# Optimization experiments

Measured on AMD Instinct MI355X. Metric: run time of the kernel, lower is better.

Reference implementation:

```python
import jax, jax.numpy as jnp
import numpy as np

BLOCK = 32


def _dct_constants(bs):
    # Replicates get_dct_constants + the sorting/reshaping done in DCTEncoderLayer.__init__
    x, y = np.meshgrid(np.arange(bs), np.arange(bs), indexing='xy')
    basis = np.zeros((bs, bs, bs, bs), dtype=np.float32)
    mag = np.zeros((bs, bs), dtype=np.float64)
    fac = np.zeros((bs, bs), dtype=np.float32)
    for v in range(bs):
        for u in range(bs):
            xb = np.cos((2 * x + 1) * u * np.pi / (2 * bs))
            yb = np.cos((2 * y + 1) * v * np.pi / (2 * bs))
            basis[v, u] = (xb * yb).astype(np.float32)
            mag[v, u] = np.linalg.norm(np.array([v, u], dtype=np.int64))
            c_v = 1 / np.sqrt(2) if v == 0 else 1.0
            c_u = 1 / np.sqrt(2) if u == 0 else 1.0
            fac[v, u] = c_u * c_v
    kernels = basis.reshape(-1, bs, bs)
    factors = fac.reshape(-1)
    idx = np.argsort(mag.reshape(-1))  # same default argsort as the torch module
    return kernels[idx].astype(np.float32), factors[idx].astype(np.float32)


def setup_inputs() -> dict:
    key = jax.random.key(0)
    rgb = jax.random.uniform(key, (32, 3, 512, 512), dtype=jnp.float32)
    kernels, factors = _dct_constants(BLOCK)
    return {
        "rgb_images_batch": rgb,
        "kernels": jnp.asarray(kernels),   # [K=bs^2, bs, bs], sorted by freq magnitude
        "factors": jnp.asarray(factors),   # [K]
    }


def _rgb_to_ycbcr(rgb):
    # kornia.color.rgb_to_ycbcr (delta = 0.5)
    r, g, b = rgb[:, 0], rgb[:, 1], rgb[:, 2]
    y = 0.299 * r + 0.587 * g + 0.114 * b
    cb = (b - y) * 0.564 + 0.5
    cr = (r - y) * 0.713 + 0.5
    return jnp.stack([y, cb, cr], axis=1)  # [B,3,H,W]


def reference(rgb_images_batch, kernels, factors):
    bs = BLOCK
    B, C, H, W = rgb_images_batch.shape
    nh, nw = H // bs, W // bs
    ycbcr = 2.0 * _rgb_to_ycbcr(rgb_images_batch) - 1.0            # [B,3,H,W]
    # non-overlapping blocks: [B,3,nh,nw,bs,bs]
    blocks = ycbcr.reshape(B, 3, nh, bs, nw, bs).transpose(0, 1, 2, 4, 3, 5)
    # stride=bs conv2d with dense DCT basis kernels == per-block contraction
    coeffs = jnp.einsum('bcmnxy,kxy->bckmn', blocks, kernels)      # [B,3,K,nh,nw]
    scale = (2.0 / bs) * factors                                   # [K]
    coeffs = coeffs * scale[None, None, :, None, None]
    # torch.cat([y, cb, cr], dim=1) -> [B, 3*K, nh, nw]
    return coeffs.reshape(B, 3 * bs * bs, nh, nw)
```

## Files before the change

kernel.cpp:

```cpp
#include <hip/hip_runtime.h>
#include <math.h>


typedef __bf16 bf16x8 __attribute__((ext_vector_type(8)));
typedef float  f32x4  __attribute__((ext_vector_type(4)));

#define PI_F 3.14159265358979323846f

__device__ __forceinline__ unsigned short f2bf(float f) {
    union { float f; unsigned u; } v; v.f = f;
    unsigned u = v.u;
    u += 0x7fffu + ((u >> 16) & 1u);
    return (unsigned short)(u >> 16);
}

__global__ __launch_bounds__(256) void setup_kernel(const float* __restrict__ kern,
                                                    const float* __restrict__ factors,
                                                    unsigned short* __restrict__ Cbf,
                                                    int* __restrict__ P,
                                                    float* __restrict__ S) {
    int k = blockIdx.x * 256 + threadIdx.x;
    int i = k & 31, t = k >> 5;
    Cbf[k] = f2bf(cosf((float)((2 * i + 1) * t) * (PI_F / 64.f)));

    float k00 = kern[(size_t)k * 1024];
    float rv  = kern[(size_t)k * 1024 + 32] / k00;
    float ru  = kern[(size_t)k * 1024 + 1]  / k00;
    float cv2 = fminf(fmaxf((rv + 3.f) * 0.25f, 0.f), 1.f);
    float cu2 = fminf(fmaxf((ru + 3.f) * 0.25f, 0.f), 1.f);
    int v = __float2int_rn(acosf(sqrtf(cv2)) * (64.f / PI_F));
    int u = __float2int_rn(acosf(sqrtf(cu2)) * (64.f / PI_F));
    P[v * 32 + u] = k;
    S[k] = factors[k] * (2.f / 32.f);
}

__global__ __launch_bounds__(512, 2) void dct_fused(const float* __restrict__ rgb,
                                                    const unsigned short* __restrict__ Cbf,
                                                    const int* __restrict__ P,
                                                    const float* __restrict__ S,
                                                    float* __restrict__ out) {
    __shared__ __align__(16) unsigned char Tls[32 * 1280];

    const int tid  = threadIdx.x;
    const int lane = tid & 63;
    const int w    = tid >> 6;
    const int quad = lane >> 4;
    const int l15  = lane & 15;
    const int b    = blockIdx.x >> 4;
    const int m    = blockIdx.x & 15;

    union { bf16x8 v; unsigned short s[8]; } af0, af1;
    af0.v = *(const bf16x8*)(Cbf + l15 * 32 + quad * 8);
    af1.v = *(const bf16x8*)(Cbf + (16 + l15) * 32 + quad * 8);

    const f32x4 zero = {0.f, 0.f, 0.f, 0.f};
    f32x4 d[3][2][4];

    const float* rbase = rgb + (size_t)b * 786432 + (size_t)l15 * 32 + (size_t)quad * 8;
#pragma unroll
    for (int xi = 0; xi < 4; ++xi) {
        const int x = w * 4 + xi;
        const float* p = rbase + (size_t)(m * 32 + x) * 512;
        float4 R0 = *(const float4*)(p);
        float4 R1 = *(const float4*)(p + 4);
        float4 G0 = *(const float4*)(p + 262144);
        float4 G1 = *(const float4*)(p + 262148);
        float4 B0 = *(const float4*)(p + 524288);
        float4 B1 = *(const float4*)(p + 524292);
        float R[8]  = {R0.x, R0.y, R0.z, R0.w, R1.x, R1.y, R1.z, R1.w};
        float G[8]  = {G0.x, G0.y, G0.z, G0.w, G1.x, G1.y, G1.z, G1.w};
        float Bv[8] = {B0.x, B0.y, B0.z, B0.w, B1.x, B1.y, B1.z, B1.w};
        union { bf16x8 v; unsigned short s[8]; } fy, fcb, fcr;
#pragma unroll
        for (int e = 0; e < 8; ++e) {
            float y = 0.299f * R[e] + 0.587f * G[e] + 0.114f * Bv[e];
            fy.s[e]  = f2bf(2.f * y - 1.f);
            fcb.s[e] = f2bf(1.128f * (Bv[e] - y));
            fcr.s[e] = f2bf(1.426f * (R[e] - y));
        }
        d[0][0][xi] = __builtin_amdgcn_mfma_f32_16x16x32_bf16(af0.v, fy.v,  zero, 0, 0, 0);
        d[0][1][xi] = __builtin_amdgcn_mfma_f32_16x16x32_bf16(af1.v, fy.v,  zero, 0, 0, 0);
        d[1][0][xi] = __builtin_amdgcn_mfma_f32_16x16x32_bf16(af0.v, fcb.v, zero, 0, 0, 0);
        d[1][1][xi] = __builtin_amdgcn_mfma_f32_16x16x32_bf16(af1.v, fcb.v, zero, 0, 0, 0);
        d[2][0][xi] = __builtin_amdgcn_mfma_f32_16x16x32_bf16(af0.v, fcr.v, zero, 0, 0, 0);
        d[2][1][xi] = __builtin_amdgcn_mfma_f32_16x16x32_bf16(af1.v, fcr.v, zero, 0, 0, 0);
    }

    const size_t obase0 = (size_t)(b * 3) * 262144 + (size_t)m * 16 + (size_t)l15;
#pragma unroll 1
    for (int c = 0; c < 3; ++c) {
#pragma unroll
        for (int fh = 0; fh < 2; ++fh)
#pragma unroll
            for (int r = 0; r < 4; ++r) {
                const int f1 = fh * 16 + quad * 4 + r;
                ushort4 pk;
                pk.x = f2bf(d[c][fh][0][r]);
                pk.y = f2bf(d[c][fh][1][r]);
                pk.z = f2bf(d[c][fh][2][r]);
                pk.w = f2bf(d[c][fh][3][r]);
                *(ushort4*)(Tls + f1 * 1280 + l15 * 80 + w * 8) = pk;
            }
        __syncthreads();

        const size_t obase = obase0 + (size_t)c * 262144;
#pragma unroll
        for (int i = 0; i < 4; ++i) {
            const int f1 = w * 4 + i;
            bf16x8 bfr = *(const bf16x8*)(Tls + f1 * 1280 + l15 * 80 + quad * 16);
#pragma unroll
            for (int uh = 0; uh < 2; ++uh) {
                f32x4 d2 = __builtin_amdgcn_mfma_f32_16x16x32_bf16(
                    uh ? af1.v : af0.v, bfr, zero, 0, 0, 0);
                const int f2b = uh * 16 + quad * 4;
#pragma unroll
                for (int r = 0; r < 4; ++r) {
                    const int kk = P[(f2b + r) * 32 + f1];
                    out[obase + (size_t)kk * 256] = d2[r] * S[kk];
                }
            }
        }
        __syncthreads();
    }
}

extern "C" void kernel_launch(void* const* d_in, const int* in_sizes, int n_in,
                              void* d_out, int out_size, void* d_ws, size_t ws_size,
                              hipStream_t stream) {
    const float* rgb     = (const float*)d_in[0];
    const float* kern    = (const float*)d_in[1];
    const float* factors = (const float*)d_in[2];
    float* out = (float*)d_out;

    unsigned short* Cbf = (unsigned short*)d_ws;
    int*   P = (int*)((char*)d_ws + 8192);
    float* S = (float*)((char*)d_ws + 12288);

    setup_kernel<<<4, 256, 0, stream>>>(kern, factors, Cbf, P, S);
    dct_fused<<<512, 512, 0, stream>>>(rgb, Cbf, P, S, out);
}
```

Baseline: 234.5 us.

## Defer first-pass MFMAs per channel, pack index/scale table, raise occupancy

The kernel now keeps the converted bf16 input fragments in registers and runs the first-pass MFMAs per channel inside the channel loop, instead of holding all 24 f32x4 accumulators live. This lowers register pressure so launch bounds can request 4 blocks per SM instead of 2. The permutation index and scale are packed into one int2 table, so each output needs one dependent load instead of two. The block-row mapping is also swizzled. The risks are more MFMA work sitting on the store path, and the shared-memory footprint limiting the extra occupancy.

```diff
diff --git a/kernel.cpp b/kernel.cpp
--- a/kernel.cpp
+++ b/kernel.cpp
@@ -17,8 +17,7 @@
 __global__ __launch_bounds__(256) void setup_kernel(const float* __restrict__ kern,
                                                     const float* __restrict__ factors,
                                                     unsigned short* __restrict__ Cbf,
-                                                    int* __restrict__ P,
-                                                    float* __restrict__ S) {
+                                                    int2* __restrict__ T2) {
     int k = blockIdx.x * 256 + threadIdx.x;
     int i = k & 31, t = k >> 5;
     Cbf[k] = f2bf(cosf((float)((2 * i + 1) * t) * (PI_F / 64.f)));
@@ -30,14 +29,13 @@
     float cu2 = fminf(fmaxf((ru + 3.f) * 0.25f, 0.f), 1.f);
     int v = __float2int_rn(acosf(sqrtf(cv2)) * (64.f / PI_F));
     int u = __float2int_rn(acosf(sqrtf(cu2)) * (64.f / PI_F));
-    P[v * 32 + u] = k;
-    S[k] = factors[k] * (2.f / 32.f);
+    float s = factors[k] * (2.f / 32.f);
+    T2[v * 32 + u] = make_int2(k, __float_as_int(s));
 }
 
-__global__ __launch_bounds__(512, 2) void dct_fused(const float* __restrict__ rgb,
+__global__ __launch_bounds__(512, 4) void dct_fused(const float* __restrict__ rgb,
                                                     const unsigned short* __restrict__ Cbf,
-                                                    const int* __restrict__ P,
-                                                    const float* __restrict__ S,
+                                                    const int2* __restrict__ T2,
                                                     float* __restrict__ out) {
     __shared__ __align__(16) unsigned char Tls[32 * 1280];
 
@@ -47,15 +45,16 @@
     const int quad = lane >> 4;
     const int l15  = lane & 15;
     const int b    = blockIdx.x >> 4;
-    const int m    = blockIdx.x & 15;
+    const int loc  = blockIdx.x & 15;
+    const int m    = ((loc & 7) << 1) | (loc >> 3);
 
     union { bf16x8 v; unsigned short s[8]; } af0, af1;
     af0.v = *(const bf16x8*)(Cbf + l15 * 32 + quad * 8);
     af1.v = *(const bf16x8*)(Cbf + (16 + l15) * 32 + quad * 8);
 
     const f32x4 zero = {0.f, 0.f, 0.f, 0.f};
-    f32x4 d[3][2][4];
 
+    bf16x8 fr[3][4];
     const float* rbase = rgb + (size_t)b * 786432 + (size_t)l15 * 32 + (size_t)quad * 8;
 #pragma unroll
     for (int xi = 0; xi < 4; ++xi) {
@@ -78,29 +77,32 @@
             fcb.s[e] = f2bf(1.128f * (Bv[e] - y));
             fcr.s[e] = f2bf(1.426f * (R[e] - y));
         }
-        d[0][0][xi] = __builtin_amdgcn_mfma_f32_16x16x32_bf16(af0.v, fy.v,  zero, 0, 0, 0);
-        d[0][1][xi] = __builtin_amdgcn_mfma_f32_16x16x32_bf16(af1.v, fy.v,  zero, 0, 0, 0);
-        d[1][0][xi] = __builtin_amdgcn_mfma_f32_16x16x32_bf16(af0.v, fcb.v, zero, 0, 0, 0);
-        d[1][1][xi] = __builtin_amdgcn_mfma_f32_16x16x32_bf16(af1.v, fcb.v, zero, 0, 0, 0);
-        d[2][0][xi] = __builtin_amdgcn_mfma_f32_16x16x32_bf16(af0.v, fcr.v, zero, 0, 0, 0);
-        d[2][1][xi] = __builtin_amdgcn_mfma_f32_16x16x32_bf16(af1.v, fcr.v, zero, 0, 0, 0);
+        fr[0][xi] = fy.v;
+        fr[1][xi] = fcb.v;
+        fr[2][xi] = fcr.v;
     }
 
     const size_t obase0 = (size_t)(b * 3) * 262144 + (size_t)m * 16 + (size_t)l15;
-#pragma unroll 1
+#pragma unroll
     for (int c = 0; c < 3; ++c) {
 #pragma unroll
-        for (int fh = 0; fh < 2; ++fh)
+        for (int fh = 0; fh < 2; ++fh) {
+            f32x4 dd[4];
+#pragma unroll
+            for (int xi = 0; xi < 4; ++xi)
+                dd[xi] = __builtin_amdgcn_mfma_f32_16x16x32_bf16(
+                    fh ? af1.v : af0.v, fr[c][xi], zero, 0, 0, 0);
 #pragma unroll
             for (int r = 0; r < 4; ++r) {
                 const int f1 = fh * 16 + quad * 4 + r;
                 ushort4 pk;
-                pk.x = f2bf(d[c][fh][0][r]);
-                pk.y = f2bf(d[c][fh][1][r]);
-                pk.z = f2bf(d[c][fh][2][r]);
-                pk.w = f2bf(d[c][fh][3][r]);
+                pk.x = f2bf(dd[0][r]);
+                pk.y = f2bf(dd[1][r]);
+                pk.z = f2bf(dd[2][r]);
+                pk.w = f2bf(dd[3][r]);
                 *(ushort4*)(Tls + f1 * 1280 + l15 * 80 + w * 8) = pk;
             }
+        }
         __syncthreads();
 
         const size_t obase = obase0 + (size_t)c * 262144;
@@ -115,8 +117,8 @@
                 const int f2b = uh * 16 + quad * 4;
 #pragma unroll
                 for (int r = 0; r < 4; ++r) {
-                    const int kk = P[(f2b + r) * 32 + f1];
-                    out[obase + (size_t)kk * 256] = d2[r] * S[kk];
+                    int2 ks = T2[(f2b + r) * 32 + f1];
+                    out[obase + (size_t)ks.x * 256] = d2[r] * __int_as_float(ks.y);
                 }
             }
         }
@@ -133,9 +135,8 @@
     float* out = (float*)d_out;
 
     unsigned short* Cbf = (unsigned short*)d_ws;
-    int*   P = (int*)((char*)d_ws + 8192);
-    float* S = (float*)((char*)d_ws + 12288);
+    int2* T2 = (int2*)((char*)d_ws + 8192);
 
-    setup_kernel<<<4, 256, 0, stream>>>(kern, factors, Cbf, P, S);
-    dct_fused<<<512, 512, 0, stream>>>(rgb, Cbf, P, S, out);
+    setup_kernel<<<4, 256, 0, stream>>>(kern, factors, Cbf, T2);
+    dct_fused<<<512, 512, 0, stream>>>(rgb, Cbf, T2, out);
 }
```

Measured after the change: 218.8 us. 6.7% less time.
